# Kernel optimization log

Hardware: AMD Instinct MI355X
Metric: run time of the kernel (lower is better)

## Reference

```python
import jax, jax.numpy as jnp
import numpy as np

B, LQ, LK = 4, 1024, 2048
DQ, DK, DV, D = 1024, 512, 512, 1024
H = 16
HD = D // H
EPS = 1e-5


def setup_inputs() -> dict:
    key = jax.random.key(0)
    ks = jax.random.split(key, 12)
    s = lambda fan: 1.0 / np.sqrt(fan)
    return {
        "query": jax.random.normal(ks[0], (B, LQ, DQ), jnp.float32),
        "key": jax.random.normal(ks[1], (B, LK, DK), jnp.float32),
        "value": jax.random.normal(ks[2], (B, LK, DV), jnp.float32),
        "key_padding_mask": jnp.ones((B, LK), jnp.int32),
        "Wq": jax.random.normal(ks[3], (DQ, D), jnp.float32) * s(DQ),
        "bq": jnp.zeros((D,), jnp.float32),
        "Wk": jax.random.normal(ks[4], (DK, D), jnp.float32) * s(DK),
        "bk": jnp.zeros((D,), jnp.float32),
        "Wv": jax.random.normal(ks[5], (DV, D), jnp.float32) * s(DV),
        "bv": jnp.zeros((D,), jnp.float32),
        "Wo": jax.random.normal(ks[6], (D, D), jnp.float32) * s(D),
        "bo": jnp.zeros((D,), jnp.float32),
        "ln_g": jnp.ones((D,), jnp.float32),
        "ln_b": jnp.zeros((D,), jnp.float32),
    }


def _layer_norm(x, g, b):
    mu = jnp.mean(x, axis=-1, keepdims=True)
    var = jnp.mean(jnp.square(x - mu), axis=-1, keepdims=True)
    return (x - mu) * jax.lax.rsqrt(var + EPS) * g + b


def reference(query, key, value, key_padding_mask, Wq, bq, Wk, bk, Wv, bv, Wo, bo, ln_g, ln_b):
    residual = query
    qn = _layer_norm(query, ln_g, ln_b)
    # projections -> [B, L, H, HD]
    q = (qn @ Wq + bq).reshape(B, LQ, H, HD)
    k = (key @ Wk + bk).reshape(B, LK, H, HD)
    v = (value @ Wv + bv).reshape(B, LK, H, HD)
    scale = HD ** -0.5
    # scores [B, H, Lq, Lk]
    scores = jnp.einsum("bqhd,bkhd->bhqk", q, k) * scale
    mask = (key_padding_mask != 0)[:, None, None, :]  # True = keep
    scores = jnp.where(mask, scores, -jnp.inf)
    attn = jax.nn.softmax(scores, axis=-1)
    # dropout is identity in eval mode
    ctx = jnp.einsum("bhqk,bkhd->bqhd", attn, v).reshape(B, LQ, D)
    out = ctx @ Wo + bo
    return out + residual
```

## Files before the change

kernel.cpp:

```cpp
#include <hip/hip_runtime.h>
#include <hip/hip_bf16.h>
#include <stdint.h>

#define Bn 4
#define LQ 1024
#define LK 2048
#define Dm 1024
#define Hn 16
#define HD 64

typedef __attribute__((ext_vector_type(4))) float f32x4;
typedef __attribute__((ext_vector_type(16))) float f32x16;
typedef __attribute__((ext_vector_type(8))) short bf16x8;

__device__ __forceinline__ ushort f2bf(float f) {
  union { float f; uint32_t u; } v; v.f = f;
  uint32_t r = v.u + 0x7FFF + ((v.u >> 16) & 1);
  return (ushort)(r >> 16);
}

__device__ __forceinline__ uint32_t cvt_pk_bf16(float lo, float hi) {
  uint32_t r;
  asm("v_cvt_pk_bf16_f32 %0, %1, %2" : "=v"(r) : "v"(lo), "v"(hi));
  return r;
}

__device__ __forceinline__ float exp2v(float x) {
  float r;
  asm("v_exp_f32 %0, %1" : "=v"(r) : "v"(x));
  return r;
}

__device__ __forceinline__ void gload16(const void* g, void* lds) {
  __builtin_amdgcn_global_load_lds(
      (const __attribute__((address_space(1))) void*)g,
      (__attribute__((address_space(3))) void*)lds, 16, 0, 0);
}

__device__ __forceinline__ void wait_vm0_barrier() {
  asm volatile("s_waitcnt vmcnt(0)" ::: "memory");
  __builtin_amdgcn_s_barrier();
}

__device__ __forceinline__ void wait_all_barrier() {
  asm volatile("s_waitcnt vmcnt(0) lgkmcnt(0)" ::: "memory");
  __builtin_amdgcn_s_barrier();
}

__device__ __forceinline__ void wait_lgkm0_barrier() {
  asm volatile("s_waitcnt lgkmcnt(0)" ::: "memory");
  __builtin_amdgcn_s_barrier();
}

__global__ __launch_bounds__(256) void transpose4_kernel(
    const float* __restrict__ Wq, ushort* __restrict__ WqT,
    const float* __restrict__ Wk, ushort* __restrict__ WkT,
    const float* __restrict__ Wv, ushort* __restrict__ WvT,
    const float* __restrict__ Wo, ushort* __restrict__ WoT) {
  __shared__ float tile[64][65];
  int id = blockIdx.x;
  const float* W; ushort* Wt; int K, N, kx, ny;
  if (id < 256)      { W = Wq; Wt = WqT; K = 1024; N = 1024; kx = id & 15; ny = id >> 4; }
  else if (id < 384) { int i = id - 256; W = Wk; Wt = WkT; K = 512; N = 1024; kx = i & 7; ny = i >> 3; }
  else if (id < 512) { int i = id - 384; W = Wv; Wt = WvT; K = 512; N = 1024; kx = i & 7; ny = i >> 3; }
  else               { int i = id - 512; W = Wo; Wt = WoT; K = 1024; N = 1024; kx = i & 15; ny = i >> 4; }
  int k0 = kx * 64, n0 = ny * 64;
  int tx = threadIdx.x & 63, ty = threadIdx.x >> 6;
#pragma unroll
  for (int i = 0; i < 16; ++i) {
    int r = ty + i * 4;
    tile[r][tx] = W[(size_t)(k0 + r) * N + n0 + tx];
  }
  __syncthreads();
#pragma unroll
  for (int i = 0; i < 16; ++i) {
    int r = ty + i * 4;
    Wt[(size_t)(n0 + r) * K + k0 + tx] = f2bf(tile[tx][r]);
  }
}

__global__ __launch_bounds__(256) void cast2_kernel(
    const float4* __restrict__ k4, ushort4* __restrict__ kb,
    const float4* __restrict__ v4, ushort4* __restrict__ vb) {
  const int n4 = (8192 * 512) / 4;
  int i = blockIdx.x * 256 + threadIdx.x;
  int stride = gridDim.x * 256;
  for (; i < 2 * n4; i += stride) {
    float4 v = (i < n4) ? k4[i] : v4[i - n4];
    ushort4 o = make_ushort4(f2bf(v.x), f2bf(v.y), f2bf(v.z), f2bf(v.w));
    if (i < n4) kb[i] = o; else vb[i - n4] = o;
  }
}

__global__ __launch_bounds__(256) void ln_kernel(
    const float* __restrict__ x, const float* __restrict__ g,
    const float* __restrict__ b, ushort* __restrict__ y) {
  int row = blockIdx.x;
  const float4* xr = (const float4*)(x + (size_t)row * 1024);
  float4 v = xr[threadIdx.x];
  float s1 = v.x + v.y + v.z + v.w;
  float s2 = v.x * v.x + v.y * v.y + v.z * v.z + v.w * v.w;
#pragma unroll
  for (int off = 32; off > 0; off >>= 1) {
    s1 += __shfl_down(s1, off);
    s2 += __shfl_down(s2, off);
  }
  __shared__ float r1[4], r2[4];
  int w = threadIdx.x >> 6, lane = threadIdx.x & 63;
  if (lane == 0) { r1[w] = s1; r2[w] = s2; }
  __syncthreads();
  s1 = r1[0] + r1[1] + r1[2] + r1[3];
  s2 = r2[0] + r2[1] + r2[2] + r2[3];
  float mu = s1 * (1.0f / 1024.0f);
  float var = s2 * (1.0f / 1024.0f) - mu * mu;
  float rstd = rsqrtf(var + 1e-5f);
  float4 gv = ((const float4*)g)[threadIdx.x];
  float4 bv = ((const float4*)b)[threadIdx.x];
  ushort4 o;
  o.x = f2bf((v.x - mu) * rstd * gv.x + bv.x);
  o.y = f2bf((v.y - mu) * rstd * gv.y + bv.y);
  o.z = f2bf((v.z - mu) * rstd * gv.z + bv.z);
  o.w = f2bf((v.w - mu) * rstd * gv.w + bv.w);
  ((ushort4*)(y + (size_t)row * 1024))[threadIdx.x] = o;
}

__global__ __launch_bounds__(512) void qkv_gemm_kernel(
    const ushort* __restrict__ qn, const ushort* __restrict__ WqT,
    const float* __restrict__ bq, ushort* __restrict__ Qb,
    const ushort* __restrict__ keyb, const ushort* __restrict__ WkT,
    const float* __restrict__ bk, ushort* __restrict__ Kb,
    const ushort* __restrict__ valb, const ushort* __restrict__ WvT,
    const float* __restrict__ bv, ushort* __restrict__ Vt, float qscale) {
  __shared__ ushort As[2][128 * 64];
  __shared__ ushort Bs[2][128 * 64];

  int o = blockIdx.x;
  int logical = (o & 7) * 160 + (o >> 3);
  int g5 = logical / 5, r5 = logical % 5;
  const ushort* A; const ushort* Bt; const float* bias; ushort* out;
  int K, bx, by, epi; float osc = 1.0f;
  if (r5 == 0) {
    A = qn; Bt = WqT; bias = bq; out = Qb; K = 1024; epi = 0;
    osc = qscale; bx = g5 & 7; by = g5 >> 3;
  } else if (r5 <= 2) {
    int i = g5 * 2 + (r5 - 1);
    A = keyb; Bt = WkT; bias = bk; out = Kb; K = 512; epi = 0;
    bx = i & 7; by = i >> 3;
  } else {
    int i = g5 * 2 + (r5 - 3);
    A = valb; Bt = WvT; bias = bv; out = Vt; K = 512; epi = 1;
    bx = i & 7; by = i >> 3;
  }
  const int N = 1024;
  const int m0 = by * 128, n0 = bx * 128;

  const int t = threadIdx.x;
  const int lane = t & 63;
  const int w = t >> 6;
  const int wm = w >> 2, wn = w & 3;
  const int l31 = lane & 31, hl = lane >> 5;

  f32x16 acc[2] = {};

  const ushort* Ap[2];
  const ushort* Bp[2];
#pragma unroll
  for (int i = 0; i < 2; ++i) {
    int c = t + i * 512;
    int r = c >> 3, x = ((c & 7) ^ (r & 7)) * 8;
    Ap[i] = A + (size_t)(m0 + r) * K + x;
    Bp[i] = Bt + (size_t)(n0 + r) * K + x;
  }

  auto stage = [&](int buf, int kt) {
    gload16(Ap[0] + kt, (char*)As[buf] + (size_t)t * 16);
    gload16(Ap[1] + kt, (char*)As[buf] + (size_t)(t + 512) * 16);
    gload16(Bp[0] + kt, (char*)Bs[buf] + (size_t)t * 16);
    gload16(Bp[1] + kt, (char*)Bs[buf] + (size_t)(t + 512) * 16);
  };

  stage(0, 0);

  int cur = 0;
  for (int kt = 0; kt < K; kt += 64) {
    if (kt + 64 < K) {
      stage(cur ^ 1, kt + 64);
      asm volatile("s_waitcnt vmcnt(4)" ::: "memory");
    } else {
      asm volatile("s_waitcnt vmcnt(0)" ::: "memory");
    }
    __builtin_amdgcn_s_barrier();

    bf16x8 af[2][4], bfr[4];
#pragma unroll
    for (int m = 0; m < 2; ++m) {
      int row = wm * 64 + m * 32 + l31;
      const char* ar = (const char*)As[cur] + row * 128;
      int rs = row & 7;
#pragma unroll
      for (int kc = 0; kc < 4; ++kc)
        af[m][kc] = *(const bf16x8*)(ar + ((kc * 2 + hl) ^ rs) * 16);
    }
    {
      int row = wn * 32 + l31;
      const char* br = (const char*)Bs[cur] + row * 128;
      int rs = row & 7;
#pragma unroll
      for (int kc = 0; kc < 4; ++kc)
        bfr[kc] = *(const bf16x8*)(br + ((kc * 2 + hl) ^ rs) * 16);
    }
#pragma unroll
    for (int kc = 0; kc < 4; ++kc)
#pragma unroll
      for (int m = 0; m < 2; ++m)
        acc[m] = __builtin_amdgcn_mfma_f32_32x32x16_bf16(af[m][kc], bfr[kc], acc[m], 0, 0, 0);

    wait_lgkm0_barrier();
    cur ^= 1;
  }

  const int col = n0 + wn * 32 + l31;
  const float bias_v = bias[col];

#pragma unroll
  for (int m = 0; m < 2; ++m) {
    int rbase = m0 + wm * 64 + m * 32 + hl * 4;
#pragma unroll
    for (int rq = 0; rq < 4; ++rq) {
      int row0 = rbase + rq * 8;
      if (epi == 1) {
        int bb = row0 >> 11;
        int key = row0 & 2047;
        int h = col >> 6, hd = col & 63;
        ushort4 pk;
        pk.x = f2bf(acc[m][rq * 4 + 0] + bias_v);
        pk.y = f2bf(acc[m][rq * 4 + 1] + bias_v);
        pk.z = f2bf(acc[m][rq * 4 + 2] + bias_v);
        pk.w = f2bf(acc[m][rq * 4 + 3] + bias_v);
        *(ushort4*)(out + ((size_t)((bb * 16 + h) * 64 + hd)) * 2048 + key) = pk;
      } else {
#pragma unroll
        for (int j = 0; j < 4; ++j) {
          int row = row0 + j;
          float v = (acc[m][rq * 4 + j] + bias_v) * osc;
          out[(size_t)row * N + col] = f2bf(v);
        }
      }
    }
  }
}

__global__ __launch_bounds__(512) void oproj_gemm_kernel(
    const ushort* __restrict__ A, const ushort* __restrict__ Bt,
    const float* __restrict__ bias, float* __restrict__ Cout,
    const float* __restrict__ residual, int M, int N, int K) {
  __shared__ ushort As[2][128 * 64];
  __shared__ ushort Bs[2][128 * 64];
  const int t = threadIdx.x;
  const int lane = t & 63;
  const int w = t >> 6;
  const int wm = w >> 2, wn = w & 3;
  const int m0 = blockIdx.y * 128, n0 = blockIdx.x * 128;
  const int l31 = lane & 31, hl = lane >> 5;

  f32x16 acc[2] = {};

  const ushort* Ap[2];
  const ushort* Bp[2];
#pragma unroll
  for (int i = 0; i < 2; ++i) {
    int c = t + i * 512;
    int r = c >> 3, x = ((c & 7) ^ (r & 7)) * 8;
    Ap[i] = A + (size_t)(m0 + r) * K + x;
    Bp[i] = Bt + (size_t)(n0 + r) * K + x;
  }

  auto stage = [&](int buf, int kt) {
    gload16(Ap[0] + kt, (char*)As[buf] + (size_t)t * 16);
    gload16(Ap[1] + kt, (char*)As[buf] + (size_t)(t + 512) * 16);
    gload16(Bp[0] + kt, (char*)Bs[buf] + (size_t)t * 16);
    gload16(Bp[1] + kt, (char*)Bs[buf] + (size_t)(t + 512) * 16);
  };

  stage(0, 0);

  int cur = 0;
  for (int kt = 0; kt < K; kt += 64) {
    if (kt + 64 < K) {
      stage(cur ^ 1, kt + 64);
      asm volatile("s_waitcnt vmcnt(4)" ::: "memory");
    } else {
      asm volatile("s_waitcnt vmcnt(0)" ::: "memory");
    }
    __builtin_amdgcn_s_barrier();

    bf16x8 af[2][4], bfr[4];
#pragma unroll
    for (int m = 0; m < 2; ++m) {
      int row = wm * 64 + m * 32 + l31;
      const char* ar = (const char*)As[cur] + row * 128;
      int rs = row & 7;
#pragma unroll
      for (int kc = 0; kc < 4; ++kc)
        af[m][kc] = *(const bf16x8*)(ar + ((kc * 2 + hl) ^ rs) * 16);
    }
    {
      int row = wn * 32 + l31;
      const char* br = (const char*)Bs[cur] + row * 128;
      int rs = row & 7;
#pragma unroll
      for (int kc = 0; kc < 4; ++kc)
        bfr[kc] = *(const bf16x8*)(br + ((kc * 2 + hl) ^ rs) * 16);
    }
#pragma unroll
    for (int kc = 0; kc < 4; ++kc)
#pragma unroll
      for (int m = 0; m < 2; ++m)
        acc[m] = __builtin_amdgcn_mfma_f32_32x32x16_bf16(af[m][kc], bfr[kc], acc[m], 0, 0, 0);

    wait_lgkm0_barrier();
    cur ^= 1;
  }

  const int col = n0 + wn * 32 + l31;
  const float bias_v = bias[col];

#pragma unroll
  for (int m = 0; m < 2; ++m) {
    int rbase = m0 + wm * 64 + m * 32 + hl * 4;
#pragma unroll
    for (int rq = 0; rq < 4; ++rq) {
      int row0 = rbase + rq * 8;
#pragma unroll
      for (int j = 0; j < 4; ++j) {
        size_t idx = (size_t)(row0 + j) * N + col;
        Cout[idx] = acc[m][rq * 4 + j] + bias_v + residual[idx];
      }
    }
  }
}

__global__ __launch_bounds__(256) void attn_kernel(
    const ushort* __restrict__ Qb, const ushort* __restrict__ Kb,
    const ushort* __restrict__ Vt, const int* __restrict__ mask,
    ushort* __restrict__ ctx) {
  __shared__ __align__(16) char smem[128 + 2 * 16384];
  int* tilevalid = (int*)smem;
  char* KsBase = smem + 128;
  char* VsBase = smem + 128 + 16384;

  const int t = threadIdx.x, lane = t & 63, w = t >> 6;
  const int l31 = lane & 31, hl = lane >> 5;
  int o = blockIdx.x;
  int logical = (o & 7) * 64 + (o >> 3);
  const int b = logical >> 7;
  const int hh = (logical >> 3) & 15;
  const int q0 = (logical & 7) * 128;
  const int* maskp = mask + b * 2048;

  const int cA = t, cB = t + 256;
  const int rA = cA >> 3, rB = cB >> 3;
  const int xA = ((cA & 7) ^ (rA & 7)) * 8, xB = ((cB & 7) ^ (rB & 7)) * 8;
  const ushort* kpA = Kb + ((size_t)(b * 2048 + rA)) * 1024 + hh * 64 + xA;
  const ushort* kpB = Kb + ((size_t)(b * 2048 + rB)) * 1024 + hh * 64 + xB;
  const ushort* vpA = Vt + ((size_t)((b * 16 + hh) * 64 + rA)) * 2048 + xA;
  const ushort* vpB = Vt + ((size_t)((b * 16 + hh) * 64 + rB)) * 2048 + xB;

  auto stageKV = [&](int buf) {
    char* kd = KsBase + buf * 8192;
    char* vd = VsBase + buf * 8192;
    gload16(kpA, kd + cA * 16);
    gload16(kpB, kd + cB * 16);
    gload16(vpA, vd + cA * 16);
    gload16(vpB, vd + cB * 16);
  };

  if (t < 32) tilevalid[t] = 1;
  __syncthreads();
  stageKV(0);
  {
    const int* mp = maskp + t * 8;
    int ok = 1;
#pragma unroll
    for (int j = 0; j < 8; ++j) ok &= (mp[j] != 0) ? 1 : 0;
    atomicAnd(&tilevalid[t >> 3], ok);
  }

  bf16x8 qf[4];
  {
    int qrow = q0 + w * 32 + l31;
    const ushort* qp = Qb + ((size_t)(b * 1024 + qrow)) * 1024 + hh * 64 + hl * 8;
    qf[0] = *(const bf16x8*)(qp);
    qf[1] = *(const bf16x8*)(qp + 16);
    qf[2] = *(const bf16x8*)(qp + 32);
    qf[3] = *(const bf16x8*)(qp + 48);
  }

  const int rs = l31 & 7;
  int lo[2][2][4];
#pragma unroll
  for (int bu = 0; bu < 2; ++bu)
#pragma unroll
    for (int r2 = 0; r2 < 2; ++r2)
#pragma unroll
      for (int kc = 0; kc < 4; ++kc)
        lo[bu][r2][kc] = 128 + bu * 8192 + (r2 * 32 + l31) * 128 + (((kc * 2 + hl) ^ rs) * 16);

  f32x16 o_acc[2] = {};
  float m_run = -1e30f, l_run = 0.0f;

  wait_all_barrier();

  auto body = [&](const int CUR, int TILE) __attribute__((always_inline)) {
    if (TILE + 1 < 32) {
      kpA += 64 * 1024; kpB += 64 * 1024; vpA += 64; vpB += 64;
      stageKV(CUR ^ 1);
    }

    f32x16 sacc[2] = {};
    __builtin_amdgcn_s_setprio(1);
#pragma unroll
    for (int kb = 0; kb < 2; ++kb)
#pragma unroll
      for (int kc = 0; kc < 4; ++kc) {
        bf16x8 kf = *(const bf16x8*)(smem + lo[CUR][kb][kc]);
        sacc[kb] = __builtin_amdgcn_mfma_f32_32x32x16_bf16(kf, qf[kc], sacc[kb], 0, 0, 0);
      }
    __builtin_amdgcn_s_setprio(0);

    int allv = __builtin_amdgcn_readfirstlane(tilevalid[TILE]);
    if (!allv) {
      const int* mrow = maskp + TILE * 64 + 4 * hl;
#pragma unroll
      for (int kb = 0; kb < 2; ++kb)
#pragma unroll
        for (int rq = 0; rq < 4; ++rq) {
          int4 mv = *(const int4*)(mrow + kb * 32 + rq * 8);
          sacc[kb][rq * 4 + 0] = mv.x ? sacc[kb][rq * 4 + 0] : -1e30f;
          sacc[kb][rq * 4 + 1] = mv.y ? sacc[kb][rq * 4 + 1] : -1e30f;
          sacc[kb][rq * 4 + 2] = mv.z ? sacc[kb][rq * 4 + 2] : -1e30f;
          sacc[kb][rq * 4 + 3] = mv.w ? sacc[kb][rq * 4 + 3] : -1e30f;
        }
    }

    float tm = fmaxf(sacc[0][0], sacc[0][1]);
#pragma unroll
    for (int r = 2; r < 16; r += 2) tm = fmaxf(fmaxf(tm, sacc[0][r]), sacc[0][r + 1]);
#pragma unroll
    for (int r = 0; r < 16; r += 2) tm = fmaxf(fmaxf(tm, sacc[1][r]), sacc[1][r + 1]);
    {
      float s1 = tm, s2 = tm;
      asm("v_permlane32_swap_b32 %0, %1" : "+v"(s1), "+v"(s2));
      tm = fmaxf(tm, hl ? s1 : s2);
    }

    if (__any(tm - m_run > 11.5f)) {
      float mn = fmaxf(m_run, tm);
      float al = exp2v(m_run - mn);
      m_run = mn;
      l_run *= al;
#pragma unroll
      for (int df = 0; df < 2; ++df)
#pragma unroll
        for (int r = 0; r < 16; ++r) o_acc[df][r] *= al;
    }

    float psA = 0.0f, psB = 0.0f;
    uint32_t cpk[2][8];
#pragma unroll
    for (int kb = 0; kb < 2; ++kb)
#pragma unroll
      for (int rr = 0; rr < 8; ++rr) {
        float pa = exp2v(sacc[kb][2 * rr] - m_run);
        float pb = exp2v(sacc[kb][2 * rr + 1] - m_run);
        psA += pa; psB += pb;
        cpk[kb][rr] = cvt_pk_bf16(pa, pb);
      }
    float psum = psA + psB;
    {
      float s1 = psum, s2 = psum;
      asm("v_permlane32_swap_b32 %0, %1" : "+v"(s1), "+v"(s2));
      psum += hl ? s1 : s2;
    }
    l_run += psum;

    __builtin_amdgcn_s_setprio(1);
#pragma unroll
    for (int ks = 0; ks < 4; ++ks) {
      const int kb = ks >> 1, ci = (ks & 1) * 4;
      uint32_t a0 = cpk[kb][ci],     b0 = cpk[kb][ci + 2];
      uint32_t a1 = cpk[kb][ci + 1], b1 = cpk[kb][ci + 3];
      asm("v_permlane32_swap_b32 %0, %1" : "+v"(a0), "+v"(b0));
      asm("v_permlane32_swap_b32 %0, %1" : "+v"(a1), "+v"(b1));
      union { uint32_t u[4]; bf16x8 v; } pb_;
      pb_.u[0] = a0; pb_.u[1] = a1; pb_.u[2] = b0; pb_.u[3] = b1;
#pragma unroll
      for (int df = 0; df < 2; ++df) {
        bf16x8 vf = *(const bf16x8*)(smem + lo[CUR][df][ks] + 16384);
        o_acc[df] = __builtin_amdgcn_mfma_f32_32x32x16_bf16(vf, pb_.v, o_acc[df], 0, 0, 0);
      }
    }
    __builtin_amdgcn_s_setprio(0);

    wait_vm0_barrier();
  };

  for (int tile = 0; tile < 32; tile += 2) {
    body(0, tile);
    body(1, tile + 1);
  }

  float inv = l_run > 0.0f ? 1.0f / l_run : 0.0f;
  char* ob = KsBase + w * 4096;
#pragma unroll
  for (int df = 0; df < 2; ++df)
#pragma unroll
    for (int rq = 0; rq < 4; ++rq) {
      ushort4 pk;
      pk.x = f2bf(o_acc[df][rq * 4 + 0] * inv);
      pk.y = f2bf(o_acc[df][rq * 4 + 1] * inv);
      pk.z = f2bf(o_acc[df][rq * 4 + 2] * inv);
      pk.w = f2bf(o_acc[df][rq * 4 + 3] * inv);
      *(ushort4*)(ob + l31 * 128 + (((df * 4 + rq) ^ (l31 & 7)) * 16) + hl * 8) = pk;
    }
  asm volatile("s_waitcnt lgkmcnt(0)" ::: "memory");
#pragma unroll
  for (int i = 0; i < 4; ++i) {
    int q = (lane >> 3) + i * 8;
    int ch = lane & 7;
    uint4 v = *(const uint4*)(ob + q * 128 + ((ch ^ (q & 7)) * 16));
    int qrow = q0 + w * 32 + q;
    *(uint4*)(ctx + ((size_t)(b * 1024 + qrow)) * 1024 + hh * 64 + ch * 8) = v;
  }
}

extern "C" void kernel_launch(void* const* d_in, const int* in_sizes, int n_in,
                              void* d_out, int out_size, void* d_ws, size_t ws_size,
                              hipStream_t stream) {
  const float* query = (const float*)d_in[0];
  const float* key   = (const float*)d_in[1];
  const float* value = (const float*)d_in[2];
  const int*   mask  = (const int*)d_in[3];
  const float* Wq = (const float*)d_in[4];
  const float* bq = (const float*)d_in[5];
  const float* Wk = (const float*)d_in[6];
  const float* bk = (const float*)d_in[7];
  const float* Wv = (const float*)d_in[8];
  const float* bv = (const float*)d_in[9];
  const float* Wo = (const float*)d_in[10];
  const float* bo = (const float*)d_in[11];
  const float* ln_g = (const float*)d_in[12];
  const float* ln_b = (const float*)d_in[13];
  float* out = (float*)d_out;

  char* p = (char*)d_ws;
  auto alloc = [&](size_t elems) { ushort* r = (ushort*)p; p += elems * 2; return r; };
  ushort* WqT  = alloc((size_t)1024 * 1024);
  ushort* WkT  = alloc((size_t)1024 * 512);
  ushort* WvT  = alloc((size_t)1024 * 512);
  ushort* WoT  = alloc((size_t)1024 * 1024);
  ushort* qn   = alloc((size_t)4096 * 1024);
  ushort* keyb = alloc((size_t)8192 * 512);
  ushort* valb = alloc((size_t)8192 * 512);
  ushort* Qb   = alloc((size_t)4096 * 1024);
  ushort* Kb   = alloc((size_t)8192 * 1024);
  ushort* Vt   = alloc((size_t)8192 * 1024);
  ushort* ctx  = alloc((size_t)4096 * 1024);
  (void)ws_size; (void)in_sizes; (void)n_in; (void)out_size;

  const float QSCALE = 0.125f * 1.44269504f;

  dim3 blk(256);
  dim3 blk5(512);
  transpose4_kernel<<<dim3(768), blk, 0, stream>>>(Wq, WqT, Wk, WkT, Wv, WvT, Wo, WoT);
  cast2_kernel<<<dim3(2048), blk, 0, stream>>>(
      (const float4*)key, (ushort4*)keyb, (const float4*)value, (ushort4*)valb);
  ln_kernel<<<dim3(4096), blk, 0, stream>>>(query, ln_g, ln_b, qn);

  qkv_gemm_kernel<<<dim3(1280), blk5, 0, stream>>>(
      qn, WqT, bq, Qb, keyb, WkT, bk, Kb, valb, WvT, bv, Vt, QSCALE);

  attn_kernel<<<dim3(512), blk, 0, stream>>>(Qb, Kb, Vt, mask, ctx);

  oproj_gemm_kernel<<<dim3(8, 32), blk5, 0, stream>>>(ctx, WoT, bo, out, query, 4096, 1024, 1024);
}
```

Baseline: 144.1 us.

## Split attention keys across two wave groups and merge partial softmax states

The attention kernel now launches 512 threads per block. Two 4-wave groups each handle half of the key sequence (1024 keys) for the same 128 queries, each with its own double-buffered K/V staging area. After the loop, the groups exchange running max and sum through shared memory, and group 1 writes its rescaled partial outputs. Group 0 then merges them, normalizes, and stores ctx. This doubles the waves per block and halves the serial key loop to hide latency, at the cost of more LDS, extra barriers and a merge step.

```diff
diff --git a/kernel.cpp b/kernel.cpp
--- a/kernel.cpp
+++ b/kernel.cpp
@@ -340,35 +340,39 @@
   }
 }
 
-__global__ __launch_bounds__(256) void attn_kernel(
+__global__ __launch_bounds__(512) void attn_kernel(
     const ushort* __restrict__ Qb, const ushort* __restrict__ Kb,
     const ushort* __restrict__ Vt, const int* __restrict__ mask,
     ushort* __restrict__ ctx) {
-  __shared__ __align__(16) char smem[128 + 2 * 16384];
+  __shared__ __align__(16) char smem[128 + 65536];
   int* tilevalid = (int*)smem;
-  char* KsBase = smem + 128;
-  char* VsBase = smem + 128 + 16384;
 
   const int t = threadIdx.x, lane = t & 63, w = t >> 6;
   const int l31 = lane & 31, hl = lane >> 5;
+  const int g2 = w >> 2;
+  const int wi = w & 3;
+  const int tg = t & 255;
   int o = blockIdx.x;
   int logical = (o & 7) * 64 + (o >> 3);
   const int b = logical >> 7;
   const int hh = (logical >> 3) & 15;
   const int q0 = (logical & 7) * 128;
+  const int key0 = g2 << 10;
   const int* maskp = mask + b * 2048;
 
-  const int cA = t, cB = t + 256;
+  char* arena = smem + 128 + g2 * 32768;
+
+  const int cA = tg, cB = tg + 256;
   const int rA = cA >> 3, rB = cB >> 3;
   const int xA = ((cA & 7) ^ (rA & 7)) * 8, xB = ((cB & 7) ^ (rB & 7)) * 8;
-  const ushort* kpA = Kb + ((size_t)(b * 2048 + rA)) * 1024 + hh * 64 + xA;
-  const ushort* kpB = Kb + ((size_t)(b * 2048 + rB)) * 1024 + hh * 64 + xB;
-  const ushort* vpA = Vt + ((size_t)((b * 16 + hh) * 64 + rA)) * 2048 + xA;
-  const ushort* vpB = Vt + ((size_t)((b * 16 + hh) * 64 + rB)) * 2048 + xB;
+  const ushort* kpA = Kb + ((size_t)(b * 2048 + key0 + rA)) * 1024 + hh * 64 + xA;
+  const ushort* kpB = Kb + ((size_t)(b * 2048 + key0 + rB)) * 1024 + hh * 64 + xB;
+  const ushort* vpA = Vt + ((size_t)((b * 16 + hh) * 64 + rA)) * 2048 + key0 + xA;
+  const ushort* vpB = Vt + ((size_t)((b * 16 + hh) * 64 + rB)) * 2048 + key0 + xB;
 
   auto stageKV = [&](int buf) {
-    char* kd = KsBase + buf * 8192;
-    char* vd = VsBase + buf * 8192;
+    char* kd = arena + buf * 8192;
+    char* vd = arena + 16384 + buf * 8192;
     gload16(kpA, kd + cA * 16);
     gload16(kpB, kd + cB * 16);
     gload16(vpA, vd + cA * 16);
@@ -379,16 +383,14 @@
   __syncthreads();
   stageKV(0);
   {
-    const int* mp = maskp + t * 8;
-    int ok = 1;
-#pragma unroll
-    for (int j = 0; j < 8; ++j) ok &= (mp[j] != 0) ? 1 : 0;
-    atomicAnd(&tilevalid[t >> 3], ok);
+    const int* mp = maskp + t * 4;
+    int ok = (mp[0] != 0) & (mp[1] != 0) & (mp[2] != 0) & (mp[3] != 0);
+    atomicAnd(&tilevalid[t >> 4], ok);
   }
 
   bf16x8 qf[4];
   {
-    int qrow = q0 + w * 32 + l31;
+    int qrow = q0 + wi * 32 + l31;
     const ushort* qp = Qb + ((size_t)(b * 1024 + qrow)) * 1024 + hh * 64 + hl * 8;
     qf[0] = *(const bf16x8*)(qp);
     qf[1] = *(const bf16x8*)(qp + 16);
@@ -404,7 +406,7 @@
     for (int r2 = 0; r2 < 2; ++r2)
 #pragma unroll
       for (int kc = 0; kc < 4; ++kc)
-        lo[bu][r2][kc] = 128 + bu * 8192 + (r2 * 32 + l31) * 128 + (((kc * 2 + hl) ^ rs) * 16);
+        lo[bu][r2][kc] = 128 + g2 * 32768 + bu * 8192 + (r2 * 32 + l31) * 128 + (((kc * 2 + hl) ^ rs) * 16);
 
   f32x16 o_acc[2] = {};
   float m_run = -1e30f, l_run = 0.0f;
@@ -412,7 +414,7 @@
   wait_all_barrier();
 
   auto body = [&](const int CUR, int TILE) __attribute__((always_inline)) {
-    if (TILE + 1 < 32) {
+    if (TILE + 1 < 16) {
       kpA += 64 * 1024; kpB += 64 * 1024; vpA += 64; vpB += 64;
       stageKV(CUR ^ 1);
     }
@@ -428,9 +430,9 @@
       }
     __builtin_amdgcn_s_setprio(0);
 
-    int allv = __builtin_amdgcn_readfirstlane(tilevalid[TILE]);
+    int allv = __builtin_amdgcn_readfirstlane(tilevalid[g2 * 16 + TILE]);
     if (!allv) {
-      const int* mrow = maskp + TILE * 64 + 4 * hl;
+      const int* mrow = maskp + key0 + TILE * 64 + 4 * hl;
 #pragma unroll
       for (int kb = 0; kb < 2; ++kb)
 #pragma unroll
@@ -505,32 +507,64 @@
     wait_vm0_barrier();
   };
 
-  for (int tile = 0; tile < 32; tile += 2) {
+  for (int tile = 0; tile < 16; tile += 2) {
     body(0, tile);
     body(1, tile + 1);
   }
 
-  float inv = l_run > 0.0f ? 1.0f / l_run : 0.0f;
-  char* ob = KsBase + w * 4096;
-#pragma unroll
-  for (int df = 0; df < 2; ++df)
-#pragma unroll
-    for (int rq = 0; rq < 4; ++rq) {
-      ushort4 pk;
-      pk.x = f2bf(o_acc[df][rq * 4 + 0] * inv);
-      pk.y = f2bf(o_acc[df][rq * 4 + 1] * inv);
-      pk.z = f2bf(o_acc[df][rq * 4 + 2] * inv);
-      pk.w = f2bf(o_acc[df][rq * 4 + 3] * inv);
-      *(ushort4*)(ob + l31 * 128 + (((df * 4 + rq) ^ (l31 & 7)) * 16) + hl * 8) = pk;
-    }
-  asm volatile("s_waitcnt lgkmcnt(0)" ::: "memory");
-#pragma unroll
-  for (int i = 0; i < 4; ++i) {
-    int q = (lane >> 3) + i * 8;
-    int ch = lane & 7;
-    uint4 v = *(const uint4*)(ob + q * 128 + ((ch ^ (q & 7)) * 16));
-    int qrow = q0 + w * 32 + q;
-    *(uint4*)(ctx + ((size_t)(b * 1024 + qrow)) * 1024 + hh * 64 + ch * 8) = v;
+  float* mlb = (float*)(smem + 128);
+  mlb[(w * 64 + lane) * 2 + 0] = m_run;
+  mlb[(w * 64 + lane) * 2 + 1] = l_run;
+  wait_lgkm0_barrier();
+  const int pwv = w ^ 4;
+  float m1 = mlb[(pwv * 64 + lane) * 2 + 0];
+  float l1 = mlb[(pwv * 64 + lane) * 2 + 1];
+  float mm = fmaxf(m_run, m1);
+  float a0 = exp2v(m_run - mm);
+  float lsum = a0 * l_run + exp2v(m1 - mm) * l1;
+
+  char* obuf = smem + 128 + 4096;
+  if (g2 == 1) {
+    char* dst = obuf + wi * 8192 + lane * 16;
+#pragma unroll
+    for (int df = 0; df < 2; ++df)
+#pragma unroll
+      for (int rq = 0; rq < 4; ++rq) {
+        f32x4 c;
+        c[0] = o_acc[df][rq * 4 + 0] * a0;
+        c[1] = o_acc[df][rq * 4 + 1] * a0;
+        c[2] = o_acc[df][rq * 4 + 2] * a0;
+        c[3] = o_acc[df][rq * 4 + 3] * a0;
+        *(f32x4*)(dst + (df * 4 + rq) * 1024) = c;
+      }
+  }
+  wait_lgkm0_barrier();
+
+  if (g2 == 0) {
+    float inv = lsum > 0.0f ? 1.0f / lsum : 0.0f;
+    const char* src = obuf + wi * 8192 + lane * 16;
+    char* ob = smem + 128 + 36864 + wi * 4096;
+#pragma unroll
+    for (int df = 0; df < 2; ++df)
+#pragma unroll
+      for (int rq = 0; rq < 4; ++rq) {
+        f32x4 c = *(const f32x4*)(src + (df * 4 + rq) * 1024);
+        ushort4 pk;
+        pk.x = f2bf((o_acc[df][rq * 4 + 0] * a0 + c[0]) * inv);
+        pk.y = f2bf((o_acc[df][rq * 4 + 1] * a0 + c[1]) * inv);
+        pk.z = f2bf((o_acc[df][rq * 4 + 2] * a0 + c[2]) * inv);
+        pk.w = f2bf((o_acc[df][rq * 4 + 3] * a0 + c[3]) * inv);
+        *(ushort4*)(ob + l31 * 128 + (((df * 4 + rq) ^ (l31 & 7)) * 16) + hl * 8) = pk;
+      }
+    asm volatile("s_waitcnt lgkmcnt(0)" ::: "memory");
+#pragma unroll
+    for (int i = 0; i < 4; ++i) {
+      int q = (lane >> 3) + i * 8;
+      int ch = lane & 7;
+      uint4 v = *(const uint4*)(ob + q * 128 + ((ch ^ (q & 7)) * 16));
+      int qrow = q0 + wi * 32 + q;
+      *(uint4*)(ctx + ((size_t)(b * 1024 + qrow)) * 1024 + hh * 64 + ch * 8) = v;
+    }
   }
 }
 
@@ -580,7 +614,7 @@
   qkv_gemm_kernel<<<dim3(1280), blk5, 0, stream>>>(
       qn, WqT, bq, Qb, keyb, WkT, bk, Kb, valb, WvT, bv, Vt, QSCALE);
 
-  attn_kernel<<<dim3(512), blk, 0, stream>>>(Qb, Kb, Vt, mask, ctx);
+  attn_kernel<<<dim3(512), blk5, 0, stream>>>(Qb, Kb, Vt, mask, ctx);
 
   oproj_gemm_kernel<<<dim3(8, 32), blk5, 0, stream>>>(ctx, WoT, bo, out, query, 4096, 1024, 1024);
 }
```

Result: no change. 144.7 us (+0.4%).

## Process two 32-row query tiles per wave to reuse K/V tiles

Applied to the files above, without the earlier changes.

Each attention workgroup now covers 256 query rows instead of 128, with every wave holding two sets of Q fragments and running two independent online-softmax states. Each K/V fragment read from LDS feeds two MFMAs, which halves global K/V staging traffic and LDS reads per query row. The grid drops from 512 to 256 workgroups, so on a GPU with about 256 CUs each CU gets one block and there is less latency hiding. Register pressure also roughly doubles for accumulators.

```diff
diff --git a/kernel.cpp b/kernel.cpp
--- a/kernel.cpp
+++ b/kernel.cpp
@@ -347,15 +347,14 @@
   __shared__ __align__(16) char smem[128 + 2 * 16384];
   int* tilevalid = (int*)smem;
   char* KsBase = smem + 128;
-  char* VsBase = smem + 128 + 16384;
 
   const int t = threadIdx.x, lane = t & 63, w = t >> 6;
   const int l31 = lane & 31, hl = lane >> 5;
   int o = blockIdx.x;
-  int logical = (o & 7) * 64 + (o >> 3);
-  const int b = logical >> 7;
-  const int hh = (logical >> 3) & 15;
-  const int q0 = (logical & 7) * 128;
+  int logical = (o & 7) * 32 + (o >> 3);
+  const int b = logical >> 6;
+  const int hh = (logical >> 2) & 15;
+  const int q0 = (logical & 3) * 256;
   const int* maskp = mask + b * 2048;
 
   const int cA = t, cB = t + 256;
@@ -368,7 +367,7 @@
 
   auto stageKV = [&](int buf) {
     char* kd = KsBase + buf * 8192;
-    char* vd = VsBase + buf * 8192;
+    char* vd = KsBase + 16384 + buf * 8192;
     gload16(kpA, kd + cA * 16);
     gload16(kpB, kd + cB * 16);
     gload16(vpA, vd + cA * 16);
@@ -386,14 +385,15 @@
     atomicAnd(&tilevalid[t >> 3], ok);
   }
 
-  bf16x8 qf[4];
-  {
-    int qrow = q0 + w * 32 + l31;
+  bf16x8 qf[2][4];
+#pragma unroll
+  for (int j = 0; j < 2; ++j) {
+    int qrow = q0 + w * 64 + j * 32 + l31;
     const ushort* qp = Qb + ((size_t)(b * 1024 + qrow)) * 1024 + hh * 64 + hl * 8;
-    qf[0] = *(const bf16x8*)(qp);
-    qf[1] = *(const bf16x8*)(qp + 16);
-    qf[2] = *(const bf16x8*)(qp + 32);
-    qf[3] = *(const bf16x8*)(qp + 48);
+    qf[j][0] = *(const bf16x8*)(qp);
+    qf[j][1] = *(const bf16x8*)(qp + 16);
+    qf[j][2] = *(const bf16x8*)(qp + 32);
+    qf[j][3] = *(const bf16x8*)(qp + 48);
   }
 
   const int rs = l31 & 7;
@@ -406,8 +406,8 @@
       for (int kc = 0; kc < 4; ++kc)
         lo[bu][r2][kc] = 128 + bu * 8192 + (r2 * 32 + l31) * 128 + (((kc * 2 + hl) ^ rs) * 16);
 
-  f32x16 o_acc[2] = {};
-  float m_run = -1e30f, l_run = 0.0f;
+  f32x16 o_acc[2][2] = {};
+  float m_run[2] = {-1e30f, -1e30f}, l_run[2] = {0.0f, 0.0f};
 
   wait_all_barrier();
 
@@ -417,14 +417,16 @@
       stageKV(CUR ^ 1);
     }
 
-    f32x16 sacc[2] = {};
+    f32x16 sacc[2][2] = {};
     __builtin_amdgcn_s_setprio(1);
 #pragma unroll
     for (int kb = 0; kb < 2; ++kb)
 #pragma unroll
       for (int kc = 0; kc < 4; ++kc) {
         bf16x8 kf = *(const bf16x8*)(smem + lo[CUR][kb][kc]);
-        sacc[kb] = __builtin_amdgcn_mfma_f32_32x32x16_bf16(kf, qf[kc], sacc[kb], 0, 0, 0);
+#pragma unroll
+        for (int j = 0; j < 2; ++j)
+          sacc[j][kb] = __builtin_amdgcn_mfma_f32_32x32x16_bf16(kf, qf[j][kc], sacc[j][kb], 0, 0, 0);
       }
     __builtin_amdgcn_s_setprio(0);
 
@@ -436,68 +438,82 @@
 #pragma unroll
         for (int rq = 0; rq < 4; ++rq) {
           int4 mv = *(const int4*)(mrow + kb * 32 + rq * 8);
-          sacc[kb][rq * 4 + 0] = mv.x ? sacc[kb][rq * 4 + 0] : -1e30f;
-          sacc[kb][rq * 4 + 1] = mv.y ? sacc[kb][rq * 4 + 1] : -1e30f;
-          sacc[kb][rq * 4 + 2] = mv.z ? sacc[kb][rq * 4 + 2] : -1e30f;
-          sacc[kb][rq * 4 + 3] = mv.w ? sacc[kb][rq * 4 + 3] : -1e30f;
+#pragma unroll
+          for (int j = 0; j < 2; ++j) {
+            sacc[j][kb][rq * 4 + 0] = mv.x ? sacc[j][kb][rq * 4 + 0] : -1e30f;
+            sacc[j][kb][rq * 4 + 1] = mv.y ? sacc[j][kb][rq * 4 + 1] : -1e30f;
+            sacc[j][kb][rq * 4 + 2] = mv.z ? sacc[j][kb][rq * 4 + 2] : -1e30f;
+            sacc[j][kb][rq * 4 + 3] = mv.w ? sacc[j][kb][rq * 4 + 3] : -1e30f;
+          }
         }
     }
 
-    float tm = fmaxf(sacc[0][0], sacc[0][1]);
-#pragma unroll
-    for (int r = 2; r < 16; r += 2) tm = fmaxf(fmaxf(tm, sacc[0][r]), sacc[0][r + 1]);
-#pragma unroll
-    for (int r = 0; r < 16; r += 2) tm = fmaxf(fmaxf(tm, sacc[1][r]), sacc[1][r + 1]);
-    {
-      float s1 = tm, s2 = tm;
+    float tm[2];
+#pragma unroll
+    for (int j = 0; j < 2; ++j) {
+      float m_ = fmaxf(sacc[j][0][0], sacc[j][0][1]);
+#pragma unroll
+      for (int r = 2; r < 16; r += 2) m_ = fmaxf(fmaxf(m_, sacc[j][0][r]), sacc[j][0][r + 1]);
+#pragma unroll
+      for (int r = 0; r < 16; r += 2) m_ = fmaxf(fmaxf(m_, sacc[j][1][r]), sacc[j][1][r + 1]);
+      float s1 = m_, s2 = m_;
       asm("v_permlane32_swap_b32 %0, %1" : "+v"(s1), "+v"(s2));
-      tm = fmaxf(tm, hl ? s1 : s2);
-    }
-
-    if (__any(tm - m_run > 11.5f)) {
-      float mn = fmaxf(m_run, tm);
-      float al = exp2v(m_run - mn);
-      m_run = mn;
-      l_run *= al;
-#pragma unroll
-      for (int df = 0; df < 2; ++df)
-#pragma unroll
-        for (int r = 0; r < 16; ++r) o_acc[df][r] *= al;
-    }
-
-    float psA = 0.0f, psB = 0.0f;
-    uint32_t cpk[2][8];
-#pragma unroll
-    for (int kb = 0; kb < 2; ++kb)
-#pragma unroll
-      for (int rr = 0; rr < 8; ++rr) {
-        float pa = exp2v(sacc[kb][2 * rr] - m_run);
-        float pb = exp2v(sacc[kb][2 * rr + 1] - m_run);
-        psA += pa; psB += pb;
-        cpk[kb][rr] = cvt_pk_bf16(pa, pb);
+      tm[j] = fmaxf(m_, hl ? s1 : s2);
+    }
+
+    if (__any(fmaxf(tm[0] - m_run[0], tm[1] - m_run[1]) > 11.5f)) {
+#pragma unroll
+      for (int j = 0; j < 2; ++j) {
+        float mn = fmaxf(m_run[j], tm[j]);
+        float al = exp2v(m_run[j] - mn);
+        m_run[j] = mn;
+        l_run[j] *= al;
+#pragma unroll
+        for (int df = 0; df < 2; ++df)
+#pragma unroll
+          for (int r = 0; r < 16; ++r) o_acc[j][df][r] *= al;
       }
-    float psum = psA + psB;
-    {
+    }
+
+    uint32_t cpk[2][2][8];
+#pragma unroll
+    for (int j = 0; j < 2; ++j) {
+      float psA = 0.0f, psB = 0.0f;
+#pragma unroll
+      for (int kb = 0; kb < 2; ++kb)
+#pragma unroll
+        for (int rr = 0; rr < 8; ++rr) {
+          float pa = exp2v(sacc[j][kb][2 * rr] - m_run[j]);
+          float pb = exp2v(sacc[j][kb][2 * rr + 1] - m_run[j]);
+          psA += pa; psB += pb;
+          cpk[j][kb][rr] = cvt_pk_bf16(pa, pb);
+        }
+      float psum = psA + psB;
       float s1 = psum, s2 = psum;
       asm("v_permlane32_swap_b32 %0, %1" : "+v"(s1), "+v"(s2));
       psum += hl ? s1 : s2;
-    }
-    l_run += psum;
+      l_run[j] += psum;
+    }
 
     __builtin_amdgcn_s_setprio(1);
 #pragma unroll
     for (int ks = 0; ks < 4; ++ks) {
       const int kb = ks >> 1, ci = (ks & 1) * 4;
-      uint32_t a0 = cpk[kb][ci],     b0 = cpk[kb][ci + 2];
-      uint32_t a1 = cpk[kb][ci + 1], b1 = cpk[kb][ci + 3];
-      asm("v_permlane32_swap_b32 %0, %1" : "+v"(a0), "+v"(b0));
-      asm("v_permlane32_swap_b32 %0, %1" : "+v"(a1), "+v"(b1));
-      union { uint32_t u[4]; bf16x8 v; } pb_;
-      pb_.u[0] = a0; pb_.u[1] = a1; pb_.u[2] = b0; pb_.u[3] = b1;
+      union { uint32_t u[4]; bf16x8 v; } pb_[2];
+#pragma unroll
+      for (int j = 0; j < 2; ++j) {
+        uint32_t a0 = cpk[j][kb][ci],     b0 = cpk[j][kb][ci + 2];
+        uint32_t a1 = cpk[j][kb][ci + 1], b1 = cpk[j][kb][ci + 3];
+        asm("v_permlane32_swap_b32 %0, %1" : "+v"(a0), "+v"(b0));
+        asm("v_permlane32_swap_b32 %0, %1" : "+v"(a1), "+v"(b1));
+        pb_[j].u[0] = a0; pb_[j].u[1] = a1; pb_[j].u[2] = b0; pb_[j].u[3] = b1;
+      }
 #pragma unroll
       for (int df = 0; df < 2; ++df) {
         bf16x8 vf = *(const bf16x8*)(smem + lo[CUR][df][ks] + 16384);
-        o_acc[df] = __builtin_amdgcn_mfma_f32_32x32x16_bf16(vf, pb_.v, o_acc[df], 0, 0, 0);
+#pragma unroll
+        for (int j = 0; j < 2; ++j)
+          o_acc[j][df] = __builtin_amdgcn_mfma_f32_32x32x16_bf16(vf, pb_[j].v, o_acc[j][df], 0, 0, 0);
       }
     }
     __builtin_amdgcn_s_setprio(0);
@@ -510,27 +526,31 @@
     body(1, tile + 1);
   }
 
-  float inv = l_run > 0.0f ? 1.0f / l_run : 0.0f;
   char* ob = KsBase + w * 4096;
 #pragma unroll
-  for (int df = 0; df < 2; ++df)
-#pragma unroll
-    for (int rq = 0; rq < 4; ++rq) {
-      ushort4 pk;
-      pk.x = f2bf(o_acc[df][rq * 4 + 0] * inv);
-      pk.y = f2bf(o_acc[df][rq * 4 + 1] * inv);
-      pk.z = f2bf(o_acc[df][rq * 4 + 2] * inv);
-      pk.w = f2bf(o_acc[df][rq * 4 + 3] * inv);
-      *(ushort4*)(ob + l31 * 128 + (((df * 4 + rq) ^ (l31 & 7)) * 16) + hl * 8) = pk;
-    }
-  asm volatile("s_waitcnt lgkmcnt(0)" ::: "memory");
-#pragma unroll
-  for (int i = 0; i < 4; ++i) {
-    int q = (lane >> 3) + i * 8;
-    int ch = lane & 7;
-    uint4 v = *(const uint4*)(ob + q * 128 + ((ch ^ (q & 7)) * 16));
-    int qrow = q0 + w * 32 + q;
-    *(uint4*)(ctx + ((size_t)(b * 1024 + qrow)) * 1024 + hh * 64 + ch * 8) = v;
+  for (int j = 0; j < 2; ++j) {
+    float inv = l_run[j] > 0.0f ? 1.0f / l_run[j] : 0.0f;
+#pragma unroll
+    for (int df = 0; df < 2; ++df)
+#pragma unroll
+      for (int rq = 0; rq < 4; ++rq) {
+        ushort4 pk;
+        pk.x = f2bf(o_acc[j][df][rq * 4 + 0] * inv);
+        pk.y = f2bf(o_acc[j][df][rq * 4 + 1] * inv);
+        pk.z = f2bf(o_acc[j][df][rq * 4 + 2] * inv);
+        pk.w = f2bf(o_acc[j][df][rq * 4 + 3] * inv);
+        *(ushort4*)(ob + l31 * 128 + (((df * 4 + rq) ^ (l31 & 7)) * 16) + hl * 8) = pk;
+      }
+    asm volatile("s_waitcnt lgkmcnt(0)" ::: "memory");
+#pragma unroll
+    for (int i = 0; i < 4; ++i) {
+      int q = (lane >> 3) + i * 8;
+      int ch = lane & 7;
+      uint4 v = *(const uint4*)(ob + q * 128 + ((ch ^ (q & 7)) * 16));
+      int qrow = q0 + w * 64 + j * 32 + q;
+      *(uint4*)(ctx + ((size_t)(b * 1024 + qrow)) * 1024 + hh * 64 + ch * 8) = v;
+    }
+    asm volatile("s_waitcnt lgkmcnt(0)" ::: "memory");
   }
 }
 
@@ -580,7 +600,7 @@
   qkv_gemm_kernel<<<dim3(1280), blk5, 0, stream>>>(
       qn, WqT, bq, Qb, keyb, WkT, bk, Kb, valb, WvT, bv, Vt, QSCALE);
 
-  attn_kernel<<<dim3(512), blk, 0, stream>>>(Qb, Kb, Vt, mask, ctx);
+  attn_kernel<<<dim3(256), blk, 0, stream>>>(Qb, Kb, Vt, mask, ctx);
 
   oproj_gemm_kernel<<<dim3(8, 32), blk5, 0, stream>>>(ctx, WoT, bo, out, query, 4096, 1024, 1024);
 }
```

New measurement: 146.8 us. No clear change (+1.9%).
